# Kernel optimization log

Measured on AMD Instinct MI355X. Metric: run time of the kernel, lower is better.

The kernel has to match this reference:

```python
import jax, jax.numpy as jnp
import numpy as np

N_NODES = 50000
N_EDGES = 800000
EPS = 1e-12  # F.normalize default eps


def spmm(edge_row, edge_col, edge_val, dense):
    # sparse [N,N] (COO edges) @ dense [N,D] -> [N,D]
    gathered = edge_val[:, None] * dense[edge_col]          # [E, D]
    return jax.ops.segment_sum(gathered, edge_row, num_segments=N_NODES)


def setup_inputs() -> dict:
    key = jax.random.key(0)
    ks = jax.random.split(key, 8)
    x = jax.random.normal(ks[0], (N_NODES, 300), dtype=jnp.float32)
    edge_row = jax.random.randint(ks[1], (N_EDGES,), 0, N_NODES, dtype=jnp.int32)
    edge_col = jax.random.randint(ks[2], (N_EDGES,), 0, N_NODES, dtype=jnp.int32)
    edge_val = jax.random.uniform(ks[3], (N_EDGES,), dtype=jnp.float32)
    W1 = jax.random.normal(ks[4], (256, 300), dtype=jnp.float32) * 0.05
    b1 = jax.random.normal(ks[5], (256,), dtype=jnp.float32) * 0.05
    W2 = jax.random.normal(ks[6], (128, 256), dtype=jnp.float32) * 0.05
    b2 = jax.random.normal(ks[7], (128,), dtype=jnp.float32) * 0.05
    return {"x": x, "edge_row": edge_row, "edge_col": edge_col,
            "edge_val": edge_val, "W1": W1, "b1": b1, "W2": W2, "b2": b2}


def reference(x, edge_row, edge_col, edge_val, W1, b1, W2, b2):
    # GraphConv 1: X @ W1.T, SpMM with adj, +bias, ReLU (dropout is eval no-op)
    h = x @ W1.T                                            # [N, 256]
    h = spmm(edge_row, edge_col, edge_val, h) + b1
    h = jax.nn.relu(h)
    # GraphConv last: no ReLU
    h = h @ W2.T                                            # [N, 128]
    h = spmm(edge_row, edge_col, edge_val, h) + b2
    # F.normalize(x): row-wise L2 normalize with eps clamp
    norm = jnp.linalg.norm(h, axis=1, keepdims=True)
    return h / jnp.maximum(norm, EPS)
```

## Files before the change

### kernel.cpp

```cpp
#include <hip/hip_runtime.h>
#include <math.h>

#define NN 50000
#define NE 800000
#define ESLICE 200192

typedef __bf16 bf16x8 __attribute__((ext_vector_type(8)));
typedef __bf16 bf16x4 __attribute__((ext_vector_type(4)));
typedef float f32x4 __attribute__((ext_vector_type(4)));

__device__ __forceinline__ void gload16(const void* g, void* l){
  __builtin_amdgcn_global_load_lds((const __attribute__((address_space(1))) void*)g,
                                   (__attribute__((address_space(3))) void*)l, 16, 0, 0);
}


__global__ void k_zero_i32(int* __restrict__ p, int n){
  int i = blockIdx.x * blockDim.x + threadIdx.x;
  if (i < n) p[i] = 0;
}

__global__ __launch_bounds__(256)
void k_rank(const int* __restrict__ erow, int* __restrict__ cnt, int* __restrict__ pos){
  const int t = blockIdx.x * 256 + threadIdx.x;
  #pragma unroll
  for (int k = 0; k < 4; ++k){
    const int e = t + k * ESLICE;
    if (e < NE){
      const int r = erow[e];
      pos[e] = atomicAdd(&cnt[r], 1);
    }
  }
}

__global__ __launch_bounds__(256)
void k_scan1(const int* __restrict__ cnt, int* __restrict__ rs, int* __restrict__ part, int n){
  const int t = threadIdx.x, b = blockIdx.x;
  const int i = b * 256 + t;
  int v = (i < n) ? cnt[i] : 0;
  const int lane = t & 63, w = t >> 6;
  int s = v;
  #pragma unroll
  for (int d = 1; d < 64; d <<= 1){ int u = __shfl_up(s, d); if (lane >= d) s += u; }
  __shared__ int wsum[4];
  if (lane == 63) wsum[w] = s;
  __syncthreads();
  int add = 0;
  #pragma unroll
  for (int k = 0; k < 4; ++k) if (k < w) add += wsum[k];
  s += add;
  if (i < n) rs[i + 1] = s;
  if (t == 255) part[b] = s;
}

__global__ __launch_bounds__(256)
void k_scan2(int* __restrict__ part, int nb){
  const int t = threadIdx.x;
  int v = (t < nb) ? part[t] : 0;
  const int lane = t & 63, w = t >> 6;
  int s = v;
  #pragma unroll
  for (int d = 1; d < 64; d <<= 1){ int u = __shfl_up(s, d); if (lane >= d) s += u; }
  __shared__ int wsum[4];
  if (lane == 63) wsum[w] = s;
  __syncthreads();
  int add = 0;
  #pragma unroll
  for (int k = 0; k < 4; ++k) if (k < w) add += wsum[k];
  s += add;
  if (t < nb) part[t] = s - v;
}

__global__ __launch_bounds__(256)
void k_scan3(int* __restrict__ rs, const int* __restrict__ part, int n){
  const int i = blockIdx.x * 256 + threadIdx.x;
  if (i < n) rs[i + 1] += part[blockIdx.x];
  if (i == 0) rs[0] = 0;
}

__global__ __launch_bounds__(256)
void k_scatter2(const int* __restrict__ erow, const int* __restrict__ ecol,
                const float* __restrict__ evalv, const int* __restrict__ rs,
                const int* __restrict__ pos, int2* __restrict__ out){
  const int t = blockIdx.x * 256 + threadIdx.x;
  #pragma unroll
  for (int k = 0; k < 4; ++k){
    const int e = t + k * ESLICE;
    if (e < NE){
      const int r = erow[e];
      const int p = rs[r] + pos[e];
      out[p] = make_int2(ecol[e], __float_as_int(evalv[e]));
    }
  }
}


__global__ __launch_bounds__(256)
void conv_bf16(const float* __restrict__ src, __bf16* __restrict__ dst,
               int M, int K, int Kp){
  const int q = blockIdx.x * 256 + threadIdx.x;
  const int perRow = Kp >> 2;
  const int r = q / perRow;
  const int k = (q - r * perRow) << 2;
  float4 v = make_float4(0.f, 0.f, 0.f, 0.f);
  if (r < M && k < K) v = *(const float4*)(src + (size_t)r * K + k);
  bf16x4 o;
  o[0] = (__bf16)v.x; o[1] = (__bf16)v.y; o[2] = (__bf16)v.z; o[3] = (__bf16)v.w;
  *(bf16x4*)(dst + (size_t)r * Kp + k) = o;
}

__global__ void k_zero_bf16(__bf16* __restrict__ p, int n4){
  int i = blockIdx.x * blockDim.x + threadIdx.x;
  if (i < n4){ bf16x4 z = {}; *(bf16x4*)(p + (size_t)i * 4) = z; }
}


template<int KT>
__global__ __launch_bounds__(256)
void gemm_bf16(const __bf16* __restrict__ A, const __bf16* __restrict__ B,
               __bf16* __restrict__ C, int ld, int N){
  __shared__ char ldsbuf[49152];
  const int tid = threadIdx.x;
  const int lane = tid & 63;
  const int bn = blockIdx.x * 64;
  const int bm = blockIdx.y * 128;
  const int wr = (tid >> 7) & 1;
  const int wc = (tid >> 6) & 1;

  f32x4 acc[4][2];
  #pragma unroll
  for (int i = 0; i < 4; ++i)
    #pragma unroll
    for (int j = 0; j < 2; ++j) acc[i][j] = (f32x4){0.f, 0.f, 0.f, 0.f};

  auto stage = [&](int kt, int sel){
    char* lb = ldsbuf + sel * 24576;
    #pragma unroll
    for (int i = 0; i < 4; ++i){
      const int d = i * 4096 + tid * 16;
      const int row = d >> 7;
      const int colb = (d & 127) ^ ((row & 7) << 4);
      const __bf16* gp = A + (size_t)(bm + row) * ld + kt * 64 + (colb >> 1);
      gload16(gp, lb + i * 4096 + (tid & 192) * 16);
    }
    #pragma unroll
    for (int i = 0; i < 2; ++i){
      const int d = i * 4096 + tid * 16;
      const int row = d >> 7;
      const int colb = (d & 127) ^ ((row & 7) << 4);
      const __bf16* gp = B + (size_t)(bn + row) * ld + kt * 64 + (colb >> 1);
      gload16(gp, lb + 16384 + i * 4096 + (tid & 192) * 16);
    }
  };

  auto compute = [&](int sel){
    const char* lA = ldsbuf + sel * 24576;
    const char* lB = lA + 16384;
    #pragma unroll
    for (int c = 0; c < 2; ++c){
      bf16x8 av[4], bv[2];
      #pragma unroll
      for (int i = 0; i < 4; ++i){
        const int row = wr * 64 + i * 16 + (lane & 15);
        const int colb = (c * 64 + ((lane >> 4) << 4)) ^ ((row & 7) << 4);
        av[i] = *(const bf16x8*)(lA + row * 128 + colb);
      }
      #pragma unroll
      for (int j = 0; j < 2; ++j){
        const int row = wc * 32 + j * 16 + (lane & 15);
        const int colb = (c * 64 + ((lane >> 4) << 4)) ^ ((row & 7) << 4);
        bv[j] = *(const bf16x8*)(lB + row * 128 + colb);
      }
      #pragma unroll
      for (int i = 0; i < 4; ++i)
        #pragma unroll
        for (int j = 0; j < 2; ++j)
          acc[i][j] = __builtin_amdgcn_mfma_f32_16x16x32_bf16(av[i], bv[j], acc[i][j], 0, 0, 0);
    }
  };

  stage(0, 0);
  for (int kt = 0; kt < KT; ++kt){
    __syncthreads();
    if (kt + 1 < KT) stage(kt + 1, (kt + 1) & 1);
    compute(kt & 1);
  }

  __syncthreads();
  float* lw = (float*)ldsbuf;
  #pragma unroll
  for (int i = 0; i < 4; ++i)
    #pragma unroll
    for (int j = 0; j < 2; ++j)
      #pragma unroll
      for (int r = 0; r < 4; ++r){
        const int row = wr * 64 + i * 16 + ((lane >> 4) << 2) + r;
        const int col = wc * 32 + j * 16 + (lane & 15);
        lw[row * 68 + col] = acc[i][j][r];
      }
  __syncthreads();
  #pragma unroll
  for (int p = 0; p < 4; ++p){
    const int row = p * 32 + (tid >> 3);
    const int col8 = (tid & 7) * 8;
    const float4 v0 = *(const float4*)&lw[row * 68 + col8];
    const float4 v1 = *(const float4*)&lw[row * 68 + col8 + 4];
    bf16x8 o;
    o[0] = (__bf16)v0.x; o[1] = (__bf16)v0.y; o[2] = (__bf16)v0.z; o[3] = (__bf16)v0.w;
    o[4] = (__bf16)v1.x; o[5] = (__bf16)v1.y; o[6] = (__bf16)v1.z; o[7] = (__bf16)v1.w;
    *(bf16x8*)(C + (size_t)(bm + row) * N + bn + col8) = o;
  }
}


__global__ __launch_bounds__(256)
void spmm_bias_relu_b16(const int2* __restrict__ ecv, const int* __restrict__ start,
                        const __bf16* __restrict__ H, const float* __restrict__ bias,
                        __bf16* __restrict__ out){
  const int w = (blockIdx.x * 256 + threadIdx.x) >> 6;
  const int lane = threadIdx.x & 63;
  const int half = lane >> 5, sl = lane & 31;
  if (w >= NN) return;
  const int s = start[w], e = start[w + 1];
  float a[8];
  #pragma unroll
  for (int k = 0; k < 8; ++k) a[k] = 0.f;
  for (int base = s; base < e; base += 64){
    int2 cv = make_int2(0, 0);
    if (base + lane < e) cv = ecv[base + lane];
    const int m = min(64, e - base);
    for (int j2 = 0; 4 * j2 < m; ++j2){
      const int idx0 = 4 * j2 + half;
      const int idx1 = idx0 + 2;
      int c0 = __shfl(cv.x, idx0);
      float v0 = __int_as_float(__shfl(cv.y, idx0));
      int c1 = __shfl(cv.x, idx1);
      float v1 = __int_as_float(__shfl(cv.y, idx1));
      if (idx0 >= m){ c0 = 0; v0 = 0.f; }
      if (idx1 >= m){ c1 = 0; v1 = 0.f; }
      const bf16x8 h0 = *(const bf16x8*)(H + (size_t)c0 * 256 + sl * 8);
      const bf16x8 h1 = *(const bf16x8*)(H + (size_t)c1 * 256 + sl * 8);
      #pragma unroll
      for (int k = 0; k < 8; ++k) a[k] = fmaf(v0, (float)h0[k], a[k]);
      #pragma unroll
      for (int k = 0; k < 8; ++k) a[k] = fmaf(v1, (float)h1[k], a[k]);
    }
  }
  #pragma unroll
  for (int k = 0; k < 8; ++k) a[k] += __shfl_xor(a[k], 32);
  const float4 b0 = *(const float4*)(bias + sl * 8);
  const float4 b1 = *(const float4*)(bias + sl * 8 + 4);
  bf16x8 o;
  o[0] = (__bf16)fmaxf(a[0] + b0.x, 0.f);
  o[1] = (__bf16)fmaxf(a[1] + b0.y, 0.f);
  o[2] = (__bf16)fmaxf(a[2] + b0.z, 0.f);
  o[3] = (__bf16)fmaxf(a[3] + b0.w, 0.f);
  o[4] = (__bf16)fmaxf(a[4] + b1.x, 0.f);
  o[5] = (__bf16)fmaxf(a[5] + b1.y, 0.f);
  o[6] = (__bf16)fmaxf(a[6] + b1.z, 0.f);
  o[7] = (__bf16)fmaxf(a[7] + b1.w, 0.f);
  if (half == 0) *(bf16x8*)(out + (size_t)w * 256 + sl * 8) = o;
}

__global__ __launch_bounds__(256)
void spmm_bias_norm_b16(const int2* __restrict__ ecv, const int* __restrict__ start,
                        const __bf16* __restrict__ H, const float* __restrict__ bias,
                        float* __restrict__ out){
  const int w = (blockIdx.x * 256 + threadIdx.x) >> 6;
  const int lane = threadIdx.x & 63;
  const int quar = lane >> 4, sl = lane & 15;
  if (w >= NN) return;
  const int s = start[w], e = start[w + 1];
  float a[8];
  #pragma unroll
  for (int k = 0; k < 8; ++k) a[k] = 0.f;
  for (int base = s; base < e; base += 64){
    int2 cv = make_int2(0, 0);
    if (base + lane < e) cv = ecv[base + lane];
    const int m = min(64, e - base);
    for (int j2 = 0; 8 * j2 < m; ++j2){
      const int idx0 = 8 * j2 + quar;
      const int idx1 = idx0 + 4;
      int c0 = __shfl(cv.x, idx0);
      float v0 = __int_as_float(__shfl(cv.y, idx0));
      int c1 = __shfl(cv.x, idx1);
      float v1 = __int_as_float(__shfl(cv.y, idx1));
      if (idx0 >= m){ c0 = 0; v0 = 0.f; }
      if (idx1 >= m){ c1 = 0; v1 = 0.f; }
      const bf16x8 h0 = *(const bf16x8*)(H + (size_t)c0 * 128 + sl * 8);
      const bf16x8 h1 = *(const bf16x8*)(H + (size_t)c1 * 128 + sl * 8);
      #pragma unroll
      for (int k = 0; k < 8; ++k) a[k] = fmaf(v0, (float)h0[k], a[k]);
      #pragma unroll
      for (int k = 0; k < 8; ++k) a[k] = fmaf(v1, (float)h1[k], a[k]);
    }
  }
  #pragma unroll
  for (int k = 0; k < 8; ++k){
    a[k] += __shfl_xor(a[k], 32);
    a[k] += __shfl_xor(a[k], 16);
  }
  const float4 b0 = *(const float4*)(bias + sl * 8);
  const float4 b1 = *(const float4*)(bias + sl * 8 + 4);
  float f[8];
  f[0] = a[0] + b0.x; f[1] = a[1] + b0.y; f[2] = a[2] + b0.z; f[3] = a[3] + b0.w;
  f[4] = a[4] + b1.x; f[5] = a[5] + b1.y; f[6] = a[6] + b1.z; f[7] = a[7] + b1.w;
  float ss = 0.f;
  #pragma unroll
  for (int k = 0; k < 8; ++k) ss = fmaf(f[k], f[k], ss);
  #pragma unroll
  for (int m2 = 1; m2 < 16; m2 <<= 1) ss += __shfl_xor(ss, m2);
  const float inv = 1.f / fmaxf(sqrtf(ss), 1e-12f);
  if (quar == 0){
    float4 o0 = make_float4(f[0] * inv, f[1] * inv, f[2] * inv, f[3] * inv);
    float4 o1 = make_float4(f[4] * inv, f[5] * inv, f[6] * inv, f[7] * inv);
    *(float4*)(out + (size_t)w * 128 + sl * 8) = o0;
    *(float4*)(out + (size_t)w * 128 + sl * 8 + 4) = o1;
  }
}


extern "C" void kernel_launch(void* const* d_in, const int* in_sizes, int n_in,
                              void* d_out, int out_size, void* d_ws, size_t ws_size,
                              hipStream_t stream){
  const float* x    = (const float*)d_in[0];
  const int*   erow = (const int*)d_in[1];
  const int*   ecol = (const int*)d_in[2];
  const float* evalv= (const float*)d_in[3];
  const float* W1   = (const float*)d_in[4];
  const float* b1   = (const float*)d_in[5];
  const float* W2   = (const float*)d_in[6];
  const float* b2   = (const float*)d_in[7];
  float* out = (float*)d_out;

  char* ws = (char*)d_ws;
  __bf16* xb  = (__bf16*)(ws);
  __bf16* W1b = (__bf16*)(ws + 32030720);
  __bf16* W2b = (__bf16*)(ws + 32194560);
  __bf16* h1  = (__bf16*)(ws + 32260096);
  __bf16* h2  = (__bf16*)(ws + 57884672);
  __bf16* h3  = (__bf16*)(ws + 83509248);
  int2*   ecv = (int2*)(ws + 96321536);
  int*    rs  = (int*)(ws + 102721536);
  int*    part= (int*)(ws + 102921552);
  int*    cur = (int*)(ws + 102922368);
  int*    pos = (int*)(ws + 32260096);

  k_zero_i32<<<196, 256, 0, stream>>>(cur, NN);
  k_rank<<<782, 256, 0, stream>>>(erow, cur, pos);
  k_scan1<<<196, 256, 0, stream>>>(cur, rs, part, NN);
  k_scan2<<<1, 256, 0, stream>>>(part, 196);
  k_scan3<<<196, 256, 0, stream>>>(rs, part, NN);
  k_scatter2<<<782, 256, 0, stream>>>(erow, ecol, evalv, rs, pos, ecv);

  conv_bf16<<<15640, 256, 0, stream>>>(x, xb, NN, 300, 320);
  conv_bf16<<<80, 256, 0, stream>>>(W1, W1b, 256, 300, 320);
  conv_bf16<<<32, 256, 0, stream>>>(W2, W2b, 128, 256, 256);

  gemm_bf16<5><<<dim3(4, 391), 256, 0, stream>>>(xb, W1b, h1, 320, 256);
  spmm_bias_relu_b16<<<12500, 256, 0, stream>>>(ecv, rs, h1, b1, h2);
  k_zero_bf16<<<12, 256, 0, stream>>>(h2 + (size_t)NN * 256, 3072);

  gemm_bf16<4><<<dim3(2, 391), 256, 0, stream>>>(h2, W2b, h3, 256, 128);
  spmm_bias_norm_b16<<<12500, 256, 0, stream>>>(ecv, rs, h3, b2, out);
}
```

Measured before the change: 210.8 us.

## Widen GEMM tiles to 128x128 and split first SpMM into channel halves

The GEMM block tile grows from 128x64 to 128x128, with each wave computing 64x64 via a 4x4 MFMA grid. The epilogue now stages bf16 instead of fp32 in LDS, which reuses A loads better and halves the grid. The first SpMM is split into two launches over 128-channel halves, with 16 lanes per row chunk and four edges processed concurrently, so each pass gathers a smaller working set of H that should stay cache-resident. The costs are higher register and LDS use (64KB, lower occupancy), fewer GEMM blocks, and reading the edge list twice.

```diff
diff --git a/kernel.cpp b/kernel.cpp
--- a/kernel.cpp
+++ b/kernel.cpp
@@ -119,22 +119,22 @@
 __global__ __launch_bounds__(256)
 void gemm_bf16(const __bf16* __restrict__ A, const __bf16* __restrict__ B,
                __bf16* __restrict__ C, int ld, int N){
-  __shared__ char ldsbuf[49152];
+  __shared__ char ldsbuf[65536];
   const int tid = threadIdx.x;
   const int lane = tid & 63;
-  const int bn = blockIdx.x * 64;
+  const int bn = blockIdx.x * 128;
   const int bm = blockIdx.y * 128;
   const int wr = (tid >> 7) & 1;
   const int wc = (tid >> 6) & 1;
 
-  f32x4 acc[4][2];
+  f32x4 acc[4][4];
   #pragma unroll
   for (int i = 0; i < 4; ++i)
     #pragma unroll
-    for (int j = 0; j < 2; ++j) acc[i][j] = (f32x4){0.f, 0.f, 0.f, 0.f};
+    for (int j = 0; j < 4; ++j) acc[i][j] = (f32x4){0.f, 0.f, 0.f, 0.f};
 
   auto stage = [&](int kt, int sel){
-    char* lb = ldsbuf + sel * 24576;
+    char* lb = ldsbuf + sel * 32768;
     #pragma unroll
     for (int i = 0; i < 4; ++i){
       const int d = i * 4096 + tid * 16;
@@ -144,7 +144,7 @@
       gload16(gp, lb + i * 4096 + (tid & 192) * 16);
     }
     #pragma unroll
-    for (int i = 0; i < 2; ++i){
+    for (int i = 0; i < 4; ++i){
       const int d = i * 4096 + tid * 16;
       const int row = d >> 7;
       const int colb = (d & 127) ^ ((row & 7) << 4);
@@ -154,11 +154,11 @@
   };
 
   auto compute = [&](int sel){
-    const char* lA = ldsbuf + sel * 24576;
+    const char* lA = ldsbuf + sel * 32768;
     const char* lB = lA + 16384;
     #pragma unroll
     for (int c = 0; c < 2; ++c){
-      bf16x8 av[4], bv[2];
+      bf16x8 av[4], bv[4];
       #pragma unroll
       for (int i = 0; i < 4; ++i){
         const int row = wr * 64 + i * 16 + (lane & 15);
@@ -166,15 +166,15 @@
         av[i] = *(const bf16x8*)(lA + row * 128 + colb);
       }
       #pragma unroll
-      for (int j = 0; j < 2; ++j){
-        const int row = wc * 32 + j * 16 + (lane & 15);
+      for (int j = 0; j < 4; ++j){
+        const int row = wc * 64 + j * 16 + (lane & 15);
         const int colb = (c * 64 + ((lane >> 4) << 4)) ^ ((row & 7) << 4);
         bv[j] = *(const bf16x8*)(lB + row * 128 + colb);
       }
       #pragma unroll
       for (int i = 0; i < 4; ++i)
         #pragma unroll
-        for (int j = 0; j < 2; ++j)
+        for (int j = 0; j < 4; ++j)
           acc[i][j] = __builtin_amdgcn_mfma_f32_16x16x32_bf16(av[i], bv[j], acc[i][j], 0, 0, 0);
     }
   };
@@ -187,39 +187,36 @@
   }
 
   __syncthreads();
-  float* lw = (float*)ldsbuf;
+  __bf16* lw = (__bf16*)ldsbuf;
   #pragma unroll
   for (int i = 0; i < 4; ++i)
     #pragma unroll
-    for (int j = 0; j < 2; ++j)
+    for (int j = 0; j < 4; ++j)
       #pragma unroll
       for (int r = 0; r < 4; ++r){
         const int row = wr * 64 + i * 16 + ((lane >> 4) << 2) + r;
-        const int col = wc * 32 + j * 16 + (lane & 15);
-        lw[row * 68 + col] = acc[i][j][r];
+        const int col = wc * 64 + j * 16 + (lane & 15);
+        lw[row * 136 + col] = (__bf16)acc[i][j][r];
       }
   __syncthreads();
   #pragma unroll
-  for (int p = 0; p < 4; ++p){
-    const int row = p * 32 + (tid >> 3);
-    const int col8 = (tid & 7) * 8;
-    const float4 v0 = *(const float4*)&lw[row * 68 + col8];
-    const float4 v1 = *(const float4*)&lw[row * 68 + col8 + 4];
-    bf16x8 o;
-    o[0] = (__bf16)v0.x; o[1] = (__bf16)v0.y; o[2] = (__bf16)v0.z; o[3] = (__bf16)v0.w;
-    o[4] = (__bf16)v1.x; o[5] = (__bf16)v1.y; o[6] = (__bf16)v1.z; o[7] = (__bf16)v1.w;
-    *(bf16x8*)(C + (size_t)(bm + row) * N + bn + col8) = o;
-  }
-}
-
-
-__global__ __launch_bounds__(256)
-void spmm_bias_relu_b16(const int2* __restrict__ ecv, const int* __restrict__ start,
-                        const __bf16* __restrict__ H, const float* __restrict__ bias,
-                        __bf16* __restrict__ out){
+  for (int p = 0; p < 8; ++p){
+    const int idx = p * 256 + tid;
+    const int row = idx >> 4;
+    const int c8 = (idx & 15) * 8;
+    const bf16x8 o = *(const bf16x8*)&lw[row * 136 + c8];
+    *(bf16x8*)(C + (size_t)(bm + row) * N + bn + c8) = o;
+  }
+}
+
+
+__global__ __launch_bounds__(256)
+void spmm_relu_half(const int2* __restrict__ ecv, const int* __restrict__ start,
+                    const __bf16* __restrict__ H, const float* __restrict__ bias,
+                    __bf16* __restrict__ out, int ch0){
   const int w = (blockIdx.x * 256 + threadIdx.x) >> 6;
   const int lane = threadIdx.x & 63;
-  const int half = lane >> 5, sl = lane & 31;
+  const int quar = lane >> 4, sl = lane & 15;
   if (w >= NN) return;
   const int s = start[w], e = start[w + 1];
   float a[8];
@@ -229,17 +226,17 @@
     int2 cv = make_int2(0, 0);
     if (base + lane < e) cv = ecv[base + lane];
     const int m = min(64, e - base);
-    for (int j2 = 0; 4 * j2 < m; ++j2){
-      const int idx0 = 4 * j2 + half;
-      const int idx1 = idx0 + 2;
+    for (int j2 = 0; 8 * j2 < m; ++j2){
+      const int idx0 = 8 * j2 + quar;
+      const int idx1 = idx0 + 4;
       int c0 = __shfl(cv.x, idx0);
       float v0 = __int_as_float(__shfl(cv.y, idx0));
       int c1 = __shfl(cv.x, idx1);
       float v1 = __int_as_float(__shfl(cv.y, idx1));
       if (idx0 >= m){ c0 = 0; v0 = 0.f; }
       if (idx1 >= m){ c1 = 0; v1 = 0.f; }
-      const bf16x8 h0 = *(const bf16x8*)(H + (size_t)c0 * 256 + sl * 8);
-      const bf16x8 h1 = *(const bf16x8*)(H + (size_t)c1 * 256 + sl * 8);
+      const bf16x8 h0 = *(const bf16x8*)(H + (size_t)c0 * 256 + ch0 + sl * 8);
+      const bf16x8 h1 = *(const bf16x8*)(H + (size_t)c1 * 256 + ch0 + sl * 8);
       #pragma unroll
       for (int k = 0; k < 8; ++k) a[k] = fmaf(v0, (float)h0[k], a[k]);
       #pragma unroll
@@ -247,9 +244,12 @@
     }
   }
   #pragma unroll
-  for (int k = 0; k < 8; ++k) a[k] += __shfl_xor(a[k], 32);
-  const float4 b0 = *(const float4*)(bias + sl * 8);
-  const float4 b1 = *(const float4*)(bias + sl * 8 + 4);
+  for (int k = 0; k < 8; ++k){
+    a[k] += __shfl_xor(a[k], 32);
+    a[k] += __shfl_xor(a[k], 16);
+  }
+  const float4 b0 = *(const float4*)(bias + ch0 + sl * 8);
+  const float4 b1 = *(const float4*)(bias + ch0 + sl * 8 + 4);
   bf16x8 o;
   o[0] = (__bf16)fmaxf(a[0] + b0.x, 0.f);
   o[1] = (__bf16)fmaxf(a[1] + b0.y, 0.f);
@@ -259,7 +259,7 @@
   o[5] = (__bf16)fmaxf(a[5] + b1.y, 0.f);
   o[6] = (__bf16)fmaxf(a[6] + b1.z, 0.f);
   o[7] = (__bf16)fmaxf(a[7] + b1.w, 0.f);
-  if (half == 0) *(bf16x8*)(out + (size_t)w * 256 + sl * 8) = o;
+  if (quar == 0) *(bf16x8*)(out + (size_t)w * 256 + ch0 + sl * 8) = o;
 }
 
 __global__ __launch_bounds__(256)
@@ -357,10 +357,11 @@
   conv_bf16<<<80, 256, 0, stream>>>(W1, W1b, 256, 300, 320);
   conv_bf16<<<32, 256, 0, stream>>>(W2, W2b, 128, 256, 256);
 
-  gemm_bf16<5><<<dim3(4, 391), 256, 0, stream>>>(xb, W1b, h1, 320, 256);
-  spmm_bias_relu_b16<<<12500, 256, 0, stream>>>(ecv, rs, h1, b1, h2);
+  gemm_bf16<5><<<dim3(2, 391), 256, 0, stream>>>(xb, W1b, h1, 320, 256);
+  spmm_relu_half<<<12500, 256, 0, stream>>>(ecv, rs, h1, b1, h2, 0);
+  spmm_relu_half<<<12500, 256, 0, stream>>>(ecv, rs, h1, b1, h2, 128);
   k_zero_bf16<<<12, 256, 0, stream>>>(h2 + (size_t)NN * 256, 3072);
 
-  gemm_bf16<4><<<dim3(2, 391), 256, 0, stream>>>(h2, W2b, h3, 256, 128);
+  gemm_bf16<4><<<dim3(1, 391), 256, 0, stream>>>(h2, W2b, h3, 256, 128);
   spmm_bias_norm_b16<<<12500, 256, 0, stream>>>(ecv, rs, h3, b2, out);
 }
```

Result: faster. 202.3 us (-4.1%).
